# Optimization experiments

Hardware: AMD Instinct MI355X
Metric: run time of the kernel (lower is better)

## Reference

```python
import jax, jax.numpy as jnp
import numpy as np

N = 100_000   # nodes
E = 1_600_000 # edges (avg degree 16)
IN = 256
OUT = 128
NEG_SLOPE = 0.01  # torch F.leaky_relu default


def setup_inputs() -> dict:
    key = jax.random.key(0)
    k1, k2, k3, k4, k5 = jax.random.split(key, 5)
    h = jax.random.normal(k1, (N, IN), dtype=jnp.float32)
    W = jax.random.normal(k2, (IN, OUT), dtype=jnp.float32) * 0.05  # fc weight (in->out)
    a = jax.random.normal(k3, (2 * OUT,), dtype=jnp.float32) * 0.05  # attn_fc weight, flattened
    src = jax.random.randint(k4, (E,), 0, N, dtype=jnp.int32)
    dst = jax.random.randint(k5, (E,), 0, N, dtype=jnp.int32)
    return {"h": h, "W": W, "a": a, "src": src, "dst": dst, "counter": 3}


def reference(h, W, a, src, dst, counter):
    out_dim = W.shape[1]
    z = h @ W                               # [N, OUT] = fc(h)
    # edge_attention: e = leaky_relu(attn_fc(cat(z[src], z[dst])))
    s = z @ a[:out_dim]                     # [N] src contribution
    t = z @ a[out_dim:]                     # [N] dst contribution
    e = jax.nn.leaky_relu(s[src] + t[dst], NEG_SLOPE)  # [E]
    # segment softmax over incoming edges of each dst node (fixed across iterations)
    m = jax.ops.segment_max(e, dst, num_segments=N)    # [N]
    w = jnp.exp(e - m[dst])                             # [E]
    denom = jax.ops.segment_sum(w, dst, num_segments=N)  # [N]
    alpha = w / denom[dst]                               # [E]
    # nodes with no in-edges keep their previous h (DGL update_all semantics)
    deg = jax.ops.segment_sum(jnp.ones_like(e), dst, num_segments=N)
    has_in = (deg > 0)[:, None]                          # [N,1]
    hcur = z
    for _ in range(int(counter)):
        agg = jax.ops.segment_sum(alpha[:, None] * hcur[src], dst, num_segments=N)  # [N,OUT]
        hcur = jnp.where(has_in, agg, hcur)
    return hcur
```

## Files before the change

kernel.cpp:

```cpp
#include <hip/hip_runtime.h>
#include <math.h>

#define IN_DIM 256
#define OUT_DIM 128
#define BK 256
#define NBMAX 512
#define CAP 5120

typedef _Float16 f16;
typedef _Float16 f16x2 __attribute__((ext_vector_type(2)));
typedef _Float16 f16x8 __attribute__((ext_vector_type(8)));
typedef float    f32x4 __attribute__((ext_vector_type(4)));

static inline size_t align256(size_t x){ return (x + 255) & ~size_t(255); }

__global__ void init_kernel(float* __restrict__ s_arr, float* __restrict__ t_arr,
                            int* __restrict__ gcursor, int N, int NB){
  int i = blockIdx.x*blockDim.x + threadIdx.x;
  int stride = gridDim.x*blockDim.x;
  for (int j=i; j<N; j+=stride){ s_arr[j] = 0.f; t_arr[j] = 0.f; }
  for (int j=i; j<NB; j+=stride) gcursor[j] = j*CAP;
}

__global__ __launch_bounds__(256) void wprep_kernel(const float* __restrict__ Wm,
    f16* __restrict__ WThi, f16* __restrict__ WTlo){
  int idx = blockIdx.x*256 + threadIdx.x;
  int k = idx >> 7, n = idx & 127;
  float v = Wm[(size_t)k*OUT_DIM + n];
  f16 hi = (f16)v;
  WThi[(size_t)n*IN_DIM + k] = hi;
  WTlo[(size_t)n*IN_DIM + k] = (f16)(v - (float)hi);
}

__global__ __launch_bounds__(256) void gemm_kernel(const float* __restrict__ h,
    const f16* __restrict__ WThi, const f16* __restrict__ WTlo,
    const float* __restrict__ attn_a,
    f16* __restrict__ zh, float* __restrict__ s_arr, float* __restrict__ t_arr, int N){
  __shared__ f16x8 Bsh[4096];
  const int t = threadIdx.x;
  const int l = t & 63;
  const int w = t >> 6;
  const int m15 = l & 15;
  const int g = l >> 4, g8 = g*8;
  const int cb = blockIdx.x & 1;
  const int rb = blockIdx.x >> 1;
  const int row0 = rb*256 + w*64;

  for (int s = t; s < 2048; s += 256){
    int seg = s >> 6;
    int j   = s & 63;
    int col = cb*64 + (seg & 3)*16 + (j & 15);
    int k   = (seg >> 2)*32 + (j >> 4)*8;
    size_t off = (size_t)col*IN_DIM + k;
    Bsh[s]        = *(const f16x8*)&WThi[off];
    Bsh[2048 + s] = *(const f16x8*)&WTlo[off];
  }

  const float* hrow[4];
  #pragma unroll
  for (int rt=0; rt<4; rt++){
    int r = row0 + rt*16 + m15;
    if (r > N-1) r = N-1;
    hrow[rt] = h + (size_t)r*IN_DIM;
  }

  f32x4 acc[4][4];
  #pragma unroll
  for (int i=0;i<4;i++)
    #pragma unroll
    for (int j2=0;j2<4;j2++) acc[i][j2] = (f32x4){0.f,0.f,0.f,0.f};

  float4 va[4], vb[4];
  f16x8 ahc[4], alc[4];
  #pragma unroll
  for (int rt=0;rt<4;rt++){
    va[rt] = *(const float4*)&hrow[rt][g8];
    vb[rt] = *(const float4*)&hrow[rt][g8+4];
  }
  #pragma unroll
  for (int rt=0;rt<4;rt++){
    float vv[8] = {va[rt].x,va[rt].y,va[rt].z,va[rt].w,
                   vb[rt].x,vb[rt].y,vb[rt].z,vb[rt].w};
    f16x8 hh, ll;
    #pragma unroll
    for (int q=0;q<8;q++){ f16 a=(f16)vv[q]; hh[q]=a; ll[q]=(f16)(vv[q]-(float)a); }
    ahc[rt]=hh; alc[rt]=ll;
  }
  __syncthreads();

  #pragma unroll
  for (int step=0; step<8; step++){
    if (step < 7){
      #pragma unroll
      for (int rt=0;rt<4;rt++){
        va[rt] = *(const float4*)&hrow[rt][(step+1)*32 + g8];
        vb[rt] = *(const float4*)&hrow[rt][(step+1)*32 + g8 + 4];
      }
    }
    #pragma unroll
    for (int ct=0; ct<4; ct++){
      f16x8 bh = Bsh[(step*4+ct)*64 + l];
      f16x8 bl = Bsh[2048 + (step*4+ct)*64 + l];
      #pragma unroll
      for (int rt=0;rt<4;rt++){
        acc[rt][ct] = __builtin_amdgcn_mfma_f32_16x16x32_f16(ahc[rt], bh, acc[rt][ct], 0, 0, 0);
        acc[rt][ct] = __builtin_amdgcn_mfma_f32_16x16x32_f16(ahc[rt], bl, acc[rt][ct], 0, 0, 0);
        acc[rt][ct] = __builtin_amdgcn_mfma_f32_16x16x32_f16(alc[rt], bh, acc[rt][ct], 0, 0, 0);
      }
    }
    if (step < 7){
      #pragma unroll
      for (int rt=0;rt<4;rt++){
        float vv[8] = {va[rt].x,va[rt].y,va[rt].z,va[rt].w,
                       vb[rt].x,vb[rt].y,vb[rt].z,vb[rt].w};
        f16x8 hh, ll;
        #pragma unroll
        for (int q=0;q<8;q++){ f16 a=(f16)vv[q]; hh[q]=a; ll[q]=(f16)(vv[q]-(float)a); }
        ahc[rt]=hh; alc[rt]=ll;
      }
    }
  }

  float as_[4], at_[4];
  #pragma unroll
  for (int ct=0; ct<4; ct++){
    as_[ct] = attn_a[cb*64 + ct*16 + m15];
    at_[ct] = attn_a[OUT_DIM + cb*64 + ct*16 + m15];
  }

  #pragma unroll
  for (int rt=0; rt<4; rt++){
    #pragma unroll
    for (int r=0; r<4; r++){
      int grow = row0 + rt*16 + g*4 + r;
      float sp = 0.f, tp = 0.f;
      #pragma unroll
      for (int ct=0; ct<4; ct++){
        float v = acc[rt][ct][r];
        if (grow < N) zh[(size_t)grow*OUT_DIM + cb*64 + ct*16 + m15] = (f16)v;
        sp = fmaf(v, as_[ct], sp);
        tp = fmaf(v, at_[ct], tp);
      }
      #pragma unroll
      for (int o=1; o<16; o<<=1){ sp += __shfl_xor(sp,o); tp += __shfl_xor(tp,o); }
      if (m15 == 0 && grow < N){
        atomicAdd(&s_arr[grow], sp);
        atomicAdd(&t_arr[grow], tp);
      }
    }
  }
}

__global__ __launch_bounds__(256) void scatter_kernel(const int* __restrict__ src,
    const int* __restrict__ dst, const float* __restrict__ s_arr,
    const float* __restrict__ t_arr, int* __restrict__ gcursor,
    int* __restrict__ p_sd, float* __restrict__ p_w, int E, int NB){
  __shared__ int lh[NBMAX];
  __shared__ int lbase[NBMAX];
  for (int i=threadIdx.x;i<NB;i+=256) lh[i]=0;
  __syncthreads();
  int base = blockIdx.x * (256*8);
  int sN[8], dN[8], rk[8];
  float wv[8];
  #pragma unroll
  for (int k=0;k<8;k++){
    int j = base + threadIdx.x + k*256;
    if (j < E){
      int s_ = src[j], d_ = dst[j];
      float e = s_arr[s_] + t_arr[d_];
      e = e > 0.f ? e : 0.01f*e;
      wv[k] = __expf(e);
      sN[k] = s_; dN[k] = d_;
      rk[k] = atomicAdd(&lh[d_>>8], 1);
    } else rk[k] = -1;
  }
  __syncthreads();
  for (int i=threadIdx.x;i<NB;i+=256){
    int c = lh[i];
    lbase[i] = c ? atomicAdd(&gcursor[i], c) : 0;
  }
  __syncthreads();
  #pragma unroll
  for (int k=0;k<8;k++){
    if (rk[k] >= 0){
      int b = dN[k] >> 8;
      int pos = lbase[b] + rk[k];
      p_sd[pos] = sN[k] | ((dN[k] & 255) << 20);
      p_w[pos]  = wv[k];
    }
  }
}

__global__ __launch_bounds__(512) void bucket_kernel(const int* __restrict__ gcursor,
    const int* __restrict__ p_sd, const float* __restrict__ p_w,
    int* __restrict__ offs_st, int* __restrict__ offs_en, int2* __restrict__ csrp,
    int N){
  __shared__ int   hist[BK];
  __shared__ float wsum[BK];
  __shared__ int   loff[BK];
  __shared__ int   wtot[4];
  int b = blockIdx.x;
  int tid = threadIdx.x;
  int e0 = b*CAP, e1 = gcursor[b];
  int n0 = b << 8;
  int nn = min(BK, N - n0);
  if (tid < BK){ hist[tid] = 0; wsum[tid] = 0.f; }
  __syncthreads();
  for (int j=e0+tid; j<e1; j+=512){
    int dl = p_sd[j] >> 20;
    atomicAdd(&hist[dl], 1);
    atomicAdd(&wsum[dl], p_w[j]);
  }
  __syncthreads();
  int lane = tid & 63, wv = tid >> 6;
  int v = (tid < BK) ? hist[tid] : 0;
  int x = v;
  #pragma unroll
  for (int o=1;o<64;o<<=1){ int y = __shfl_up(x,o); if (lane>=o) x += y; }
  if (tid < BK && lane==63) wtot[wv] = x;
  __syncthreads();
  if (tid < BK){
    int woff = 0;
    for (int i=0;i<wv;i++) woff += wtot[i];
    int excl = woff + x - v;
    if (tid < nn){
      offs_st[n0 + tid] = e0 + excl;
      offs_en[n0 + tid] = e0 + excl + v;
    }
    loff[tid] = excl;
  }
  __syncthreads();
  for (int j=e0+tid; j<e1; j+=512){
    int sd = p_sd[j];
    int dl = sd >> 20;
    int r = atomicAdd(&loff[dl], 1);
    int2 pk; pk.x = sd & 0xFFFFF; pk.y = __float_as_int(p_w[j] / wsum[dl]);
    csrp[e0 + r] = pk;
  }
}

__global__ __launch_bounds__(256) void agg_kernel(const f16* __restrict__ hIn,
    f16* __restrict__ hOut, float* __restrict__ out,
    const int* __restrict__ offs_st, const int* __restrict__ offs_en,
    const int2* __restrict__ csrp, const int* __restrict__ counter, int it, int N){
  int wv   = threadIdx.x >> 6;
  int lane = threadIdx.x & 63;
  int qg   = lane >> 4;
  int f8   = (lane & 15) * 8;
  int n = blockIdx.x*4 + wv;
  if (n >= N) return;
  int cntr = counter[0];
  if (cntr <= 0){
    if (it == 0 && qg == 0){
      f16x8 v = *(const f16x8*)&hIn[(size_t)n*OUT_DIM + f8];
      float4 o0, o1;
      o0.x=(float)v[0]; o0.y=(float)v[1]; o0.z=(float)v[2]; o0.w=(float)v[3];
      o1.x=(float)v[4]; o1.y=(float)v[5]; o1.z=(float)v[6]; o1.w=(float)v[7];
      *(float4*)&out[(size_t)n*OUT_DIM + f8]     = o0;
      *(float4*)&out[(size_t)n*OUT_DIM + f8 + 4] = o1;
    }
    return;
  }
  if (it >= cntr) return;
  const bool fin = (it == cntr - 1);
  int s0 = offs_st[n], s1 = offs_en[n];
  if (s0 == s1){
    if (qg == 0){
      f16x8 v = *(const f16x8*)&hIn[(size_t)n*OUT_DIM + f8];
      if (fin){
        float4 o0, o1;
        o0.x=(float)v[0]; o0.y=(float)v[1]; o0.z=(float)v[2]; o0.w=(float)v[3];
        o1.x=(float)v[4]; o1.y=(float)v[5]; o1.z=(float)v[6]; o1.w=(float)v[7];
        *(float4*)&out[(size_t)n*OUT_DIM + f8]     = o0;
        *(float4*)&out[(size_t)n*OUT_DIM + f8 + 4] = o1;
      } else {
        *(f16x8*)&hOut[(size_t)n*OUT_DIM + f8] = v;
      }
    }
    return;
  }
  float acc[8];
  #pragma unroll
  for (int j=0;j<8;j++) acc[j] = 0.f;

  for (int base = s0; base < s1; base += 64){
    int cnt = min(64, s1 - base);
    int2 me = make_int2(0, 0);
    if (lane < cnt) me = csrp[base + lane];
    int kmax = (cnt + 3) >> 2;
    int k = 0;
    for (; k+4 <= kmax; k += 4){
      int e0i = 4*k + qg,      e1i = 4*k+4 + qg;
      int e2i = 4*k+8 + qg,    e3i = 4*k+12 + qg;
      int   s0i = __shfl(me.x, e0i); float w0 = __int_as_float(__shfl(me.y, e0i));
      int   s1i = __shfl(me.x, e1i); float w1 = __int_as_float(__shfl(me.y, e1i));
      int   s2i = __shfl(me.x, e2i); float w2 = __int_as_float(__shfl(me.y, e2i));
      int   s3i = __shfl(me.x, e3i); float w3 = __int_as_float(__shfl(me.y, e3i));
      f16x8 v0 = *(const f16x8*)&hIn[(size_t)s0i*OUT_DIM + f8];
      f16x8 v1 = *(const f16x8*)&hIn[(size_t)s1i*OUT_DIM + f8];
      f16x8 v2 = *(const f16x8*)&hIn[(size_t)s2i*OUT_DIM + f8];
      f16x8 v3 = *(const f16x8*)&hIn[(size_t)s3i*OUT_DIM + f8];
      #pragma unroll
      for (int j=0;j<8;j++){
        acc[j] = fmaf(w0, (float)v0[j], acc[j]);
        acc[j] = fmaf(w1, (float)v1[j], acc[j]);
        acc[j] = fmaf(w2, (float)v2[j], acc[j]);
        acc[j] = fmaf(w3, (float)v3[j], acc[j]);
      }
    }
    for (; k < kmax; k++){
      int e = 4*k + qg;
      int   sk = __shfl(me.x, e);
      float wk = __int_as_float(__shfl(me.y, e));
      f16x8 v = *(const f16x8*)&hIn[(size_t)sk*OUT_DIM + f8];
      #pragma unroll
      for (int j=0;j<8;j++) acc[j] = fmaf(wk, (float)v[j], acc[j]);
    }
  }
  #pragma unroll
  for (int j=0;j<8;j++){
    acc[j] += __shfl_xor(acc[j], 16);
    acc[j] += __shfl_xor(acc[j], 32);
  }
  if (qg == 0){
    if (fin){
      float4 o0, o1;
      o0.x=acc[0]; o0.y=acc[1]; o0.z=acc[2]; o0.w=acc[3];
      o1.x=acc[4]; o1.y=acc[5]; o1.z=acc[6]; o1.w=acc[7];
      *(float4*)&out[(size_t)n*OUT_DIM + f8]     = o0;
      *(float4*)&out[(size_t)n*OUT_DIM + f8 + 4] = o1;
    } else {
      f16x8 o;
      #pragma unroll
      for (int j=0;j<8;j++) o[j] = (f16)acc[j];
      *(f16x8*)&hOut[(size_t)n*OUT_DIM + f8] = o;
    }
  }
}

extern "C" void kernel_launch(void* const* d_in, const int* in_sizes, int n_in,
                              void* d_out, int out_size, void* d_ws, size_t ws_size,
                              hipStream_t stream){
  const float* h   = (const float*)d_in[0];
  const float* Wm  = (const float*)d_in[1];
  const float* a   = (const float*)d_in[2];
  const int*   src = (const int*)d_in[3];
  const int*   dst = (const int*)d_in[4];
  const int* counter = (const int*)d_in[5];
  const int N = in_sizes[0] / IN_DIM;
  const int E = in_sizes[3];
  const int NB = (N + BK - 1) / BK;
  float* out = (float*)d_out;

  char* p = (char*)d_ws;
  auto alloc = [&](size_t bytes){ void* r = (void*)p; p += align256(bytes); return r; };
  f16*   hA        = (f16*)  alloc((size_t)N*OUT_DIM*2);
  f16*   hB        = (f16*)  alloc((size_t)N*OUT_DIM*2);
  float* s_arr     = (float*)alloc((size_t)N*4);
  float* t_arr     = (float*)alloc((size_t)N*4);
  int*   p_sd      = (int*)  alloc((size_t)NB*CAP*4);
  float* p_w       = (float*)alloc((size_t)NB*CAP*4);
  int2*  csrp      = (int2*) alloc((size_t)NB*CAP*8);
  int*   offs_st   = (int*)  alloc((size_t)N*4);
  int*   offs_en   = (int*)  alloc((size_t)N*4);
  int*   gcursor   = (int*)  alloc((size_t)NBMAX*4);
  f16*   WThi      = (f16*)  alloc((size_t)IN_DIM*OUT_DIM*2);
  f16*   WTlo      = (f16*)  alloc((size_t)IN_DIM*OUT_DIM*2);

  init_kernel<<<256, 256, 0, stream>>>(s_arr, t_arr, gcursor, N, NB);
  wprep_kernel<<<(IN_DIM*OUT_DIM)/256, 256, 0, stream>>>(Wm, WThi, WTlo);
  gemm_kernel<<<((N+255)/256)*2, 256, 0, stream>>>(h, WThi, WTlo, a, hA, s_arr, t_arr, N);
  scatter_kernel<<<(E + 2047)/2048, 256, 0, stream>>>(src, dst, s_arr, t_arr,
                                                      gcursor, p_sd, p_w, E, NB);
  bucket_kernel<<<NB, 512, 0, stream>>>(gcursor, p_sd, p_w, offs_st, offs_en, csrp, N);
  agg_kernel<<<(N+3)/4, 256, 0, stream>>>(hA, hB, out, offs_st, offs_en, csrp, counter, 0, N);
  agg_kernel<<<(N+3)/4, 256, 0, stream>>>(hB, hA, out, offs_st, offs_en, csrp, counter, 1, N);
  agg_kernel<<<(N+3)/4, 256, 0, stream>>>(hA, hB, out, offs_st, offs_en, csrp, counter, 2, N);
}
```

Before: 308.8 us.

## Rewrite GEMM as persistent kernel with register-resident W and LDS double-buffered h tiles

Rewrites the projection GEMM as a persistent kernel of 512 blocks with 512 threads each. Every wave keeps its 16-column slice of the split-f16 weights in registers, and 32-row tiles of h are staged into an XOR-swizzled, double-buffered LDS area with global_load_lds async copies, so the next tile's load overlaps the current tile's MFMAs. Each block now covers all 128 output columns, so h is read once instead of twice (the old grid split columns across two blocks). The cost is smaller MFMA tiles per wave, one barrier per tile and more atomics per row for s/t.

Result: slower. 317.9 us (+2.9%).

```diff
diff --git a/kernel.cpp b/kernel.cpp
--- a/kernel.cpp
+++ b/kernel.cpp
@@ -32,122 +32,111 @@
   WTlo[(size_t)n*IN_DIM + k] = (f16)(v - (float)hi);
 }
 
-__global__ __launch_bounds__(256) void gemm_kernel(const float* __restrict__ h,
+__global__ __launch_bounds__(512, 4) void gemm_kernel(const float* __restrict__ h,
     const f16* __restrict__ WThi, const f16* __restrict__ WTlo,
     const float* __restrict__ attn_a,
     f16* __restrict__ zh, float* __restrict__ s_arr, float* __restrict__ t_arr, int N){
-  __shared__ f16x8 Bsh[4096];
+  __shared__ float Ash[2][32*256];
   const int t = threadIdx.x;
   const int l = t & 63;
   const int w = t >> 6;
   const int m15 = l & 15;
-  const int g = l >> 4, g8 = g*8;
-  const int cb = blockIdx.x & 1;
-  const int rb = blockIdx.x >> 1;
-  const int row0 = rb*256 + w*64;
-
-  for (int s = t; s < 2048; s += 256){
-    int seg = s >> 6;
-    int j   = s & 63;
-    int col = cb*64 + (seg & 3)*16 + (j & 15);
-    int k   = (seg >> 2)*32 + (j >> 4)*8;
-    size_t off = (size_t)col*IN_DIM + k;
-    Bsh[s]        = *(const f16x8*)&WThi[off];
-    Bsh[2048 + s] = *(const f16x8*)&WTlo[off];
-  }
-
-  const float* hrow[4];
-  #pragma unroll
-  for (int rt=0; rt<4; rt++){
-    int r = row0 + rt*16 + m15;
-    if (r > N-1) r = N-1;
-    hrow[rt] = h + (size_t)r*IN_DIM;
-  }
-
-  f32x4 acc[4][4];
-  #pragma unroll
-  for (int i=0;i<4;i++)
+  const int g = l >> 4;
+  const int col = w*16 + m15;
+
+  f16x8 Bh[8], Bl[8];
+  {
+    const f16* bh = WThi + (size_t)col*IN_DIM;
+    const f16* bl = WTlo + (size_t)col*IN_DIM;
     #pragma unroll
-    for (int j2=0;j2<4;j2++) acc[i][j2] = (f32x4){0.f,0.f,0.f,0.f};
-
-  float4 va[4], vb[4];
-  f16x8 ahc[4], alc[4];
-  #pragma unroll
-  for (int rt=0;rt<4;rt++){
-    va[rt] = *(const float4*)&hrow[rt][g8];
-    vb[rt] = *(const float4*)&hrow[rt][g8+4];
-  }
-  #pragma unroll
-  for (int rt=0;rt<4;rt++){
-    float vv[8] = {va[rt].x,va[rt].y,va[rt].z,va[rt].w,
-                   vb[rt].x,vb[rt].y,vb[rt].z,vb[rt].w};
-    f16x8 hh, ll;
+    for (int s=0;s<8;s++){
+      Bh[s] = *(const f16x8*)&bh[s*32 + g*8];
+      Bl[s] = *(const f16x8*)&bl[s*32 + g*8];
+    }
+  }
+  const float a_s = attn_a[col];
+  const float a_t = attn_a[OUT_DIM + col];
+
+  const int ntiles = (N + 31) >> 5;
+  const int myrow = w*4;
+
+  auto stage = [&](int buf, int tt){
+    if (((tt+1) << 5) <= N){
+      #pragma unroll
+      for (int i=0;i<4;i++){
+        int r = myrow + i;
+        const float* rp = h + ((size_t)tt*32 + r)*IN_DIM;
+        const float* gp = rp + ((l ^ (r & 7)) << 2);
+        __builtin_amdgcn_global_load_lds(
+            (__attribute__((address_space(1))) const unsigned*)gp,
+            (__attribute__((address_space(3))) unsigned*)&Ash[buf][r*256],
+            16, 0, 0);
+      }
+    } else {
+      #pragma unroll
+      for (int i=0;i<4;i++){
+        int idx = i*512 + t;
+        int r = idx >> 6, k4 = idx & 63;
+        int grow = tt*32 + r;
+        float4 v = make_float4(0.f,0.f,0.f,0.f);
+        if (grow < N) v = *(const float4*)&h[(size_t)grow*IN_DIM + (k4<<2)];
+        *(float4*)&Ash[buf][r*256 + ((k4 ^ (r & 7)) << 2)] = v;
+      }
+    }
+  };
+
+  int tile = blockIdx.x;
+  if (tile < ntiles) stage(0, tile);
+  __syncthreads();
+  int buf = 0;
+  for (; tile < ntiles; tile += 512){
+    int nxt = tile + 512;
+    if (nxt < ntiles) stage(buf^1, nxt);
+
+    f32x4 acc0 = (f32x4){0.f,0.f,0.f,0.f};
+    f32x4 acc1 = (f32x4){0.f,0.f,0.f,0.f};
     #pragma unroll
-    for (int q=0;q<8;q++){ f16 a=(f16)vv[q]; hh[q]=a; ll[q]=(f16)(vv[q]-(float)a); }
-    ahc[rt]=hh; alc[rt]=ll;
-  }
-  __syncthreads();
-
-  #pragma unroll
-  for (int step=0; step<8; step++){
-    if (step < 7){
-      #pragma unroll
-      for (int rt=0;rt<4;rt++){
-        va[rt] = *(const float4*)&hrow[rt][(step+1)*32 + g8];
-        vb[rt] = *(const float4*)&hrow[rt][(step+1)*32 + g8 + 4];
-      }
-    }
-    #pragma unroll
-    for (int ct=0; ct<4; ct++){
-      f16x8 bh = Bsh[(step*4+ct)*64 + l];
-      f16x8 bl = Bsh[2048 + (step*4+ct)*64 + l];
-      #pragma unroll
-      for (int rt=0;rt<4;rt++){
-        acc[rt][ct] = __builtin_amdgcn_mfma_f32_16x16x32_f16(ahc[rt], bh, acc[rt][ct], 0, 0, 0);
-        acc[rt][ct] = __builtin_amdgcn_mfma_f32_16x16x32_f16(ahc[rt], bl, acc[rt][ct], 0, 0, 0);
-        acc[rt][ct] = __builtin_amdgcn_mfma_f32_16x16x32_f16(alc[rt], bh, acc[rt][ct], 0, 0, 0);
-      }
-    }
-    if (step < 7){
-      #pragma unroll
-      for (int rt=0;rt<4;rt++){
-        float vv[8] = {va[rt].x,va[rt].y,va[rt].z,va[rt].w,
-                       vb[rt].x,vb[rt].y,vb[rt].z,vb[rt].w};
+    for (int s=0;s<8;s++){
+      #pragma unroll
+      for (int rt=0;rt<2;rt++){
+        int row = rt*16 + m15;
+        int q0 = s*32 + g*8;
+        int swz = (row & 7) << 2;
+        float4 v0 = *(const float4*)&Ash[buf][row*256 + ( q0      ^ swz)];
+        float4 v1 = *(const float4*)&Ash[buf][row*256 + ((q0 + 4) ^ swz)];
+        float vv[8] = {v0.x,v0.y,v0.z,v0.w, v1.x,v1.y,v1.z,v1.w};
         f16x8 hh, ll;
         #pragma unroll
         for (int q=0;q<8;q++){ f16 a=(f16)vv[q]; hh[q]=a; ll[q]=(f16)(vv[q]-(float)a); }
-        ahc[rt]=hh; alc[rt]=ll;
-      }
-    }
-  }
-
-  float as_[4], at_[4];
-  #pragma unroll
-  for (int ct=0; ct<4; ct++){
-    as_[ct] = attn_a[cb*64 + ct*16 + m15];
-    at_[ct] = attn_a[OUT_DIM + cb*64 + ct*16 + m15];
-  }
-
-  #pragma unroll
-  for (int rt=0; rt<4; rt++){
+        if (rt == 0){
+          acc0 = __builtin_amdgcn_mfma_f32_16x16x32_f16(hh, Bh[s], acc0, 0, 0, 0);
+          acc0 = __builtin_amdgcn_mfma_f32_16x16x32_f16(hh, Bl[s], acc0, 0, 0, 0);
+          acc0 = __builtin_amdgcn_mfma_f32_16x16x32_f16(ll, Bh[s], acc0, 0, 0, 0);
+        } else {
+          acc1 = __builtin_amdgcn_mfma_f32_16x16x32_f16(hh, Bh[s], acc1, 0, 0, 0);
+          acc1 = __builtin_amdgcn_mfma_f32_16x16x32_f16(hh, Bl[s], acc1, 0, 0, 0);
+          acc1 = __builtin_amdgcn_mfma_f32_16x16x32_f16(ll, Bh[s], acc1, 0, 0, 0);
+        }
+      }
+    }
     #pragma unroll
-    for (int r=0; r<4; r++){
-      int grow = row0 + rt*16 + g*4 + r;
-      float sp = 0.f, tp = 0.f;
-      #pragma unroll
-      for (int ct=0; ct<4; ct++){
-        float v = acc[rt][ct][r];
-        if (grow < N) zh[(size_t)grow*OUT_DIM + cb*64 + ct*16 + m15] = (f16)v;
-        sp = fmaf(v, as_[ct], sp);
-        tp = fmaf(v, at_[ct], tp);
-      }
-      #pragma unroll
-      for (int o=1; o<16; o<<=1){ sp += __shfl_xor(sp,o); tp += __shfl_xor(tp,o); }
-      if (m15 == 0 && grow < N){
-        atomicAdd(&s_arr[grow], sp);
-        atomicAdd(&t_arr[grow], tp);
-      }
-    }
+    for (int rt=0;rt<2;rt++){
+      #pragma unroll
+      for (int r=0;r<4;r++){
+        int grow = tile*32 + rt*16 + g*4 + r;
+        float v = (rt==0) ? acc0[r] : acc1[r];
+        if (grow < N) zh[(size_t)grow*OUT_DIM + col] = (f16)v;
+        float sp = v * a_s, tp = v * a_t;
+        #pragma unroll
+        for (int o=1;o<16;o<<=1){ sp += __shfl_xor(sp,o); tp += __shfl_xor(tp,o); }
+        if (m15 == 0 && grow < N){
+          atomicAdd(&s_arr[grow], sp);
+          atomicAdd(&t_arr[grow], tp);
+        }
+      }
+    }
+    __syncthreads();
+    buf ^= 1;
   }
 }
 
@@ -369,7 +358,7 @@
 
   init_kernel<<<256, 256, 0, stream>>>(s_arr, t_arr, gcursor, N, NB);
   wprep_kernel<<<(IN_DIM*OUT_DIM)/256, 256, 0, stream>>>(Wm, WThi, WTlo);
-  gemm_kernel<<<((N+255)/256)*2, 256, 0, stream>>>(h, WThi, WTlo, a, hA, s_arr, t_arr, N);
+  gemm_kernel<<<512, 512, 0, stream>>>(h, WThi, WTlo, a, hA, s_arr, t_arr, N);
   scatter_kernel<<<(E + 2047)/2048, 256, 0, stream>>>(src, dst, s_arr, t_arr,
                                                       gcursor, p_sd, p_w, E, NB);
   bucket_kernel<<<NB, 512, 0, stream>>>(gcursor, p_sd, p_w, offs_st, offs_en, csrp, N);
```
